# Kernel optimization log

Measured on AMD Instinct MI355X. Metric: run time of the kernel, lower is better.

## Reference

```python
import jax, jax.numpy as jnp
import numpy as np

WS = 7
HEADS = 8
DIM = 256
IN_DIM = 128
HID = 1024
EPS = 1e-5


def _rel_index(ws):
    coords = np.stack(np.meshgrid(np.arange(ws), np.arange(ws), indexing='ij'))  # (2,ws,ws)
    cf = coords.reshape(2, -1)                      # (2,N)
    rel = (cf[:, :, None] - cf[:, None, :]).transpose(1, 2, 0).copy()  # (N,N,2)
    rel[..., 0] += ws - 1
    rel[..., 1] += ws - 1
    rel[..., 0] *= 2 * ws - 1
    return rel.sum(-1)  # (N,N) int

REL_IDX = jnp.asarray(_rel_index(WS).reshape(-1))


def layernorm(x, g, b):
    mu = jnp.mean(x, axis=-1, keepdims=True)
    var = jnp.mean(jnp.square(x - mu), axis=-1, keepdims=True)
    return (x - mu) * jax.lax.rsqrt(var + EPS) * g + b


def setup_inputs() -> dict:
    key = jax.random.key(0)
    ks = jax.random.split(key, 16)
    s = 0.02
    return {
        'x': jax.random.normal(ks[0], (16, IN_DIM, 56, 56), jnp.float32),
        'conv_w': jax.random.normal(ks[1], (DIM, IN_DIM, 3, 3), jnp.float32) * s,
        'conv_b': jnp.zeros((DIM,), jnp.float32),
        'g1': jnp.ones((DIM,), jnp.float32), 'b1': jnp.zeros((DIM,), jnp.float32),
        'g2': jnp.ones((DIM,), jnp.float32), 'b2': jnp.zeros((DIM,), jnp.float32),
        'g3': jnp.ones((DIM,), jnp.float32), 'b3': jnp.zeros((DIM,), jnp.float32),
        'qkv_w': jax.random.normal(ks[2], (3 * DIM, DIM), jnp.float32) * s,
        'rel_bias_table': jax.random.normal(ks[3], ((2 * WS - 1) ** 2, HEADS), jnp.float32) * s,
        'proj_w': jax.random.normal(ks[4], (DIM, DIM), jnp.float32) * s,
        'proj_b': jnp.zeros((DIM,), jnp.float32),
        'fc1_w': jax.random.normal(ks[5], (HID, DIM), jnp.float32) * s,
        'fc1_b': jnp.zeros((HID,), jnp.float32),
        'fc2_w': jax.random.normal(ks[6], (DIM, HID), jnp.float32) * s,
        'fc2_b': jnp.zeros((DIM,), jnp.float32),
    }


def reference(x, conv_w, conv_b, g1, b1, g2, b2, g3, b3, qkv_w, rel_bias_table,
              proj_w, proj_b, fc1_w, fc1_b, fc2_w, fc2_b):
    # proj_q: 3x3 conv, stride 1, pad 1 (input_dim != embed_dim)
    x = jax.lax.conv_general_dilated(
        x, conv_w, window_strides=(1, 1), padding=((1, 1), (1, 1)),
        dimension_numbers=('NCHW', 'OIHW', 'NCHW')) + conv_b[None, :, None, None]
    b, c, h, w = x.shape
    x = x.reshape(b, c, h * w).transpose(0, 2, 1)  # (b, n, c)
    x = layernorm(x, g1, b1)
    x = x.reshape(b, h, w, c)
    pb = (WS - h % WS) % WS
    pr = (WS - w % WS) % WS
    x = jnp.pad(x, ((0, 0), (0, pb), (0, pr), (0, 0)))
    hp, wp = h + pb, w + pr
    # window partition -> (nW, N, c)
    xw = x.reshape(b, hp // WS, WS, wp // WS, WS, c)
    xw = xw.transpose(0, 1, 3, 2, 4, 5).reshape(-1, WS * WS, c)
    nW, N, _ = xw.shape
    d = c // HEADS
    qkv = (xw @ qkv_w.T).reshape(nW, N, 3, HEADS, d).transpose(2, 0, 3, 1, 4)  # (3,nW,h,N,d)
    q, k, v = qkv[0] * (d ** -0.5), qkv[1], qkv[2]
    attn = jnp.einsum('whnd,whmd->whnm', q, k)
    bias = rel_bias_table[REL_IDX].reshape(N, N, HEADS).transpose(2, 0, 1)  # (h,N,N)
    attn = jax.nn.softmax(attn + bias[None], axis=-1)
    out = jnp.einsum('whnm,whmd->whnd', attn, v).transpose(0, 2, 1, 3).reshape(nW, N, c)
    out = out @ proj_w.T + proj_b
    # window reverse
    x = out.reshape(b, hp // WS, wp // WS, WS, WS, c)
    x = x.transpose(0, 1, 3, 2, 4, 5).reshape(b, hp, wp, c)
    x = x[:, :h, :w, :].reshape(b, h * w, c)
    # NOTE: faithful to source — NO residual from pre-attention stream
    x = layernorm(x, g2, b2)
    x = jax.nn.gelu(x @ fc1_w.T + fc1_b, approximate=False) @ fc2_w.T + fc2_b
    x = x + x  # source: x = x + drop_path(x) with identity drop_path
    x = layernorm(x, g3, b3)
    return x.reshape(b, h, w, c).transpose(0, 3, 1, 2)
```

## Files before the change

### kernel.cpp

```cpp
#include <hip/hip_runtime.h>
#include <hip/hip_bf16.h>

typedef unsigned short u16;
typedef unsigned int   u32;

#define TTOK  50176
#define CDIM  256

using short8 = __attribute__((ext_vector_type(8))) short;
using f32x4  = __attribute__((ext_vector_type(4))) float;

__device__ __forceinline__ float b2f(u16 u) { return __uint_as_float(((u32)u) << 16); }
__device__ __forceinline__ u16 f2b(float f) {
    u32 x = __float_as_uint(f);
    return (u16)((x + 0x7fffu + ((x >> 16) & 1u)) >> 16);
}

#define GLD16(src, dst) __builtin_amdgcn_global_load_lds( \
    (const __attribute__((address_space(1))) void*)(src),  \
    (__attribute__((address_space(3))) void*)(dst), 16, 0, 0)

__global__ __launch_bounds__(256) void cvt4_k(const float* __restrict__ a, const float* __restrict__ b,
                                              const float* __restrict__ c, const float* __restrict__ d,
                                              u16* __restrict__ dst) {
    int i = blockIdx.x * 256 + threadIdx.x;
    const float* src; int off;
    if (i < 49152)       { src = a; off = i; }
    else if (i < 65536)  { src = b; off = i - 49152; }
    else if (i < 131072) { src = c; off = i - 65536; }
    else                 { src = d; off = i - 131072; }
    float4 v = *(const float4*)&src[off * 4];
    ushort4 o;
    o.x = f2b(v.x); o.y = f2b(v.y); o.z = f2b(v.z); o.w = f2b(v.w);
    *(ushort4*)&dst[i * 4] = o;
}

__global__ __launch_bounds__(256) void pad_k(const float* __restrict__ x, u16* __restrict__ xp) {
    __shared__ float tile[128][58];
    int bid = blockIdx.x;
    int b = bid / 58, hp = bid - b * 58;
    int tid = threadIdx.x;
    bool zrow = (hp == 0 || hp == 57);
    if (!zrow) {
        int h = hp - 1;
        for (int e = tid; e < 128 * 14; e += 256) {
            int ic = e / 14, j = e - ic * 14;
            float4 v = *(const float4*)&x[(((size_t)b * 128 + ic) * 56 + h) * 56 + j * 4];
            tile[ic][j * 4 + 0] = v.x; tile[ic][j * 4 + 1] = v.y;
            tile[ic][j * 4 + 2] = v.z; tile[ic][j * 4 + 3] = v.w;
        }
        __syncthreads();
    }
    size_t rb = ((size_t)b * 58 + hp) * 58 * 128;
    for (int u = tid; u < 58 * 16; u += 256) {
        int wp = u / 16, icg = u - wp * 16;
        uint4 o = make_uint4(0u, 0u, 0u, 0u);
        if (!zrow && wp != 0 && wp != 57) {
            int w = wp - 1, ic0 = icg * 8;
            u16 v0 = f2b(tile[ic0 + 0][w]), v1 = f2b(tile[ic0 + 1][w]);
            u16 v2 = f2b(tile[ic0 + 2][w]), v3 = f2b(tile[ic0 + 3][w]);
            u16 v4 = f2b(tile[ic0 + 4][w]), v5 = f2b(tile[ic0 + 5][w]);
            u16 v6 = f2b(tile[ic0 + 6][w]), v7 = f2b(tile[ic0 + 7][w]);
            o.x = (u32)v0 | ((u32)v1 << 16);
            o.y = (u32)v2 | ((u32)v3 << 16);
            o.z = (u32)v4 | ((u32)v5 << 16);
            o.w = (u32)v6 | ((u32)v7 << 16);
        }
        *(uint4*)&xp[rb + (size_t)wp * 128 + icg * 8] = o;
    }
}

__global__ __launch_bounds__(256) void w2_k(const float* __restrict__ w, u16* __restrict__ o2) {
    int e = blockIdx.x * 256 + threadIdx.x;
    int o = e / 1152, rem = e - o * 1152;
    int tap = rem >> 7, ic = rem & 127;
    o2[e] = f2b(w[(o * 128 + ic) * 9 + tap]);
}

__device__ __forceinline__ void xcd_remap(int& bx, int& by) {
    int nx = gridDim.x, ny = gridDim.y;
    if ((ny & 7) == 0) {
        int linear = blockIdx.y * nx + blockIdx.x;
        int xcd = linear & 7, within = linear >> 3;
        bx = within % nx;
        by = xcd * (ny >> 3) + within / nx;
    } else { bx = blockIdx.x; by = blockIdx.y; }
}

__device__ __forceinline__ int xcd_remap1d() {
    int nb = gridDim.x, lin = blockIdx.x;
    int q = nb >> 3, r = nb & 7;
    int xcd = lin & 7, idx = lin >> 3;
    return (xcd < r ? xcd * (q + 1) : r * (q + 1) + (xcd - r) * q) + idx;
}

__global__ __launch_bounds__(256) void gemm_conv_ln_k(const u16* __restrict__ xp, const u16* __restrict__ W2,
                                                      const float* __restrict__ bias,
                                                      const float* __restrict__ gam, const float* __restrict__ bet,
                                                      u16* __restrict__ C) {
    __shared__ __align__(16) u16 lsA[64 * 64];
    __shared__ __align__(16) u16 lsB[256 * 64];
    int tid = threadIdx.x;
    int wave = tid >> 6, lane = tid & 63;
    int by = xcd_remap1d();
    int mBase = by * 64;
    int wm = wave >> 1, wn = wave & 1;
    int lr = lane & 15, lq = lane >> 4;
    int r8 = lane >> 3, kg = lane & 7;
    int kgsw = ((kg ^ r8) & 7) * 8;

    size_t tb[2]; const u16* gB[8];
#pragma unroll
    for (int j = 0; j < 2; ++j) {
        int t = mBase + wave * 16 + j * 8 + r8;
        int win = t / 49, n = t - win * 49;
        int b = win >> 6, wh = (win >> 3) & 7, ww = win & 7;
        int r = n / 7, s = n - r * 7;
        tb[j] = ((size_t)(b * 58 + wh * 7 + r) * 58 + ww * 7 + s) * 128 + kgsw;
    }
#pragma unroll
    for (int j = 0; j < 8; ++j)
        gB[j] = W2 + (size_t)(wave * 64 + j * 8 + r8) * 1152 + kgsw;

    f32x4 acc[2][8];
#pragma unroll
    for (int m = 0; m < 2; ++m)
#pragma unroll
        for (int n = 0; n < 8; ++n) acc[m][n] = (f32x4){0.f, 0.f, 0.f, 0.f};

    for (int ks = 0; ks < 18; ++ks) {
        int tap = ks >> 1, half = ks & 1;
        int kh = tap / 3, kw = tap - kh * 3;
        int uoff = (kh * 58 + kw) * 128 + half * 64;
#pragma unroll
        for (int j = 0; j < 2; ++j) GLD16(xp + tb[j] + uoff, lsA + (wave * 16 + j * 8) * 64);
#pragma unroll
        for (int j = 0; j < 8; ++j) GLD16(gB[j] + ks * 64, lsB + (wave * 64 + j * 8) * 64);
        __syncthreads();
#pragma unroll
        for (int kk = 0; kk < 2; ++kk) {
            int sl = (((kk << 2) | lq) ^ (lr & 7)) * 8;
            short8 af[2], bf[8];
#pragma unroll
            for (int m = 0; m < 2; ++m)
                af[m] = *(const short8*)&lsA[(wm * 32 + m * 16 + lr) * 64 + sl];
#pragma unroll
            for (int n = 0; n < 8; ++n)
                bf[n] = *(const short8*)&lsB[(wn * 128 + n * 16 + lr) * 64 + sl];
#pragma unroll
            for (int m = 0; m < 2; ++m)
#pragma unroll
                for (int n = 0; n < 8; ++n)
                    acc[m][n] = __builtin_amdgcn_mfma_f32_16x16x32_bf16(af[m], bf[n], acc[m][n], 0, 0, 0);
        }
        __syncthreads();
    }

    float bv[8], gv[8], btv[8];
#pragma unroll
    for (int n = 0; n < 8; ++n) {
        int col = wn * 128 + n * 16 + lr;
        bv[n] = bias[col]; gv[n] = gam[col]; btv[n] = bet[col];
    }
#pragma unroll
    for (int m = 0; m < 2; ++m)
#pragma unroll
        for (int n = 0; n < 8; ++n)
#pragma unroll
            for (int r = 0; r < 4; ++r) acc[m][n][r] += bv[n];

    float* red = (float*)lsA;
#pragma unroll
    for (int m = 0; m < 2; ++m)
#pragma unroll
        for (int r = 0; r < 4; ++r) {
            float s = 0.f, qq = 0.f;
#pragma unroll
            for (int n = 0; n < 8; ++n) { float v = acc[m][n][r]; s += v; qq += v * v; }
            s += __shfl_xor(s, 1); s += __shfl_xor(s, 2); s += __shfl_xor(s, 4); s += __shfl_xor(s, 8);
            qq += __shfl_xor(qq, 1); qq += __shfl_xor(qq, 2); qq += __shfl_xor(qq, 4); qq += __shfl_xor(qq, 8);
            if (lr == 0) {
                int row = wm * 32 + m * 16 + lq * 4 + r;
                red[row * 4 + wn * 2] = s; red[row * 4 + wn * 2 + 1] = qq;
            }
        }
    __syncthreads();

#pragma unroll
    for (int m = 0; m < 2; ++m)
#pragma unroll
        for (int r = 0; r < 4; ++r) {
            int row = wm * 32 + m * 16 + lq * 4 + r;
            float S = red[row * 4] + red[row * 4 + 2];
            float Q = red[row * 4 + 1] + red[row * 4 + 3];
            float mean = S * (1.f / 256.f);
            float var = Q * (1.f / 256.f) - mean * mean;
            float inv = rsqrtf(var + 1e-5f);
            size_t grow = (size_t)(mBase + row) * 256;
#pragma unroll
            for (int n = 0; n < 8; ++n) {
                int col = wn * 128 + n * 16 + lr;
                C[grow + col] = f2b((acc[m][n][r] - mean) * inv * gv[n] + btv[n]);
            }
        }
}

__global__ __launch_bounds__(256) void gemm_ln_k(const u16* __restrict__ A, const u16* __restrict__ Bw,
                                                 const float* __restrict__ bias,
                                                 const float* __restrict__ gam, const float* __restrict__ bet,
                                                 u16* __restrict__ C, int K) {
    __shared__ __align__(16) u16 lsA[64 * 64];
    __shared__ __align__(16) u16 lsB[256 * 64];
    int tid = threadIdx.x;
    int wave = tid >> 6, lane = tid & 63;
    int by = xcd_remap1d();
    int mBase = by * 64;
    int wm = wave >> 1, wn = wave & 1;
    int lr = lane & 15, lq = lane >> 4;
    int r8 = lane >> 3, kg = lane & 7;
    int kgsw = ((kg ^ r8) & 7) * 8;

    const u16* gA[2]; const u16* gB[8];
#pragma unroll
    for (int j = 0; j < 2; ++j)
        gA[j] = A + (size_t)(mBase + wave * 16 + j * 8 + r8) * K + kgsw;
#pragma unroll
    for (int j = 0; j < 8; ++j)
        gB[j] = Bw + (size_t)(wave * 64 + j * 8 + r8) * K + kgsw;

    f32x4 acc[2][8];
#pragma unroll
    for (int m = 0; m < 2; ++m)
#pragma unroll
        for (int n = 0; n < 8; ++n) acc[m][n] = (f32x4){0.f, 0.f, 0.f, 0.f};

    for (int k0 = 0; k0 < K; k0 += 64) {
#pragma unroll
        for (int j = 0; j < 2; ++j) GLD16(gA[j] + k0, lsA + (wave * 16 + j * 8) * 64);
#pragma unroll
        for (int j = 0; j < 8; ++j) GLD16(gB[j] + k0, lsB + (wave * 64 + j * 8) * 64);
        __syncthreads();
#pragma unroll
        for (int kk = 0; kk < 2; ++kk) {
            int sl = (((kk << 2) | lq) ^ (lr & 7)) * 8;
            short8 af[2], bf[8];
#pragma unroll
            for (int m = 0; m < 2; ++m)
                af[m] = *(const short8*)&lsA[(wm * 32 + m * 16 + lr) * 64 + sl];
#pragma unroll
            for (int n = 0; n < 8; ++n)
                bf[n] = *(const short8*)&lsB[(wn * 128 + n * 16 + lr) * 64 + sl];
#pragma unroll
            for (int m = 0; m < 2; ++m)
#pragma unroll
                for (int n = 0; n < 8; ++n)
                    acc[m][n] = __builtin_amdgcn_mfma_f32_16x16x32_bf16(af[m], bf[n], acc[m][n], 0, 0, 0);
        }
        __syncthreads();
    }

    float bv[8], gv[8], btv[8];
#pragma unroll
    for (int n = 0; n < 8; ++n) {
        int col = wn * 128 + n * 16 + lr;
        bv[n] = bias[col]; gv[n] = gam[col]; btv[n] = bet[col];
    }
#pragma unroll
    for (int m = 0; m < 2; ++m)
#pragma unroll
        for (int n = 0; n < 8; ++n)
#pragma unroll
            for (int r = 0; r < 4; ++r) acc[m][n][r] += bv[n];

    float* red = (float*)lsA;
#pragma unroll
    for (int m = 0; m < 2; ++m)
#pragma unroll
        for (int r = 0; r < 4; ++r) {
            float s = 0.f, qq = 0.f;
#pragma unroll
            for (int n = 0; n < 8; ++n) { float v = acc[m][n][r]; s += v; qq += v * v; }
            s += __shfl_xor(s, 1); s += __shfl_xor(s, 2); s += __shfl_xor(s, 4); s += __shfl_xor(s, 8);
            qq += __shfl_xor(qq, 1); qq += __shfl_xor(qq, 2); qq += __shfl_xor(qq, 4); qq += __shfl_xor(qq, 8);
            if (lr == 0) {
                int row = wm * 32 + m * 16 + lq * 4 + r;
                red[row * 4 + wn * 2] = s; red[row * 4 + wn * 2 + 1] = qq;
            }
        }
    __syncthreads();

#pragma unroll
    for (int m = 0; m < 2; ++m)
#pragma unroll
        for (int r = 0; r < 4; ++r) {
            int row = wm * 32 + m * 16 + lq * 4 + r;
            float S = red[row * 4] + red[row * 4 + 2];
            float Q = red[row * 4 + 1] + red[row * 4 + 3];
            float mean = S * (1.f / 256.f);
            float var = Q * (1.f / 256.f) - mean * mean;
            float inv = rsqrtf(var + 1e-5f);
            size_t grow = (size_t)(mBase + row) * 256;
#pragma unroll
            for (int n = 0; n < 8; ++n) {
                int col = wn * 128 + n * 16 + lr;
                C[grow + col] = f2b((acc[m][n][r] - mean) * inv * gv[n] + btv[n]);
            }
        }
}

template <int EPI>
__global__ __launch_bounds__(256) void gemm_k(const u16* __restrict__ A, const u16* __restrict__ Bw,
                                              const float* __restrict__ bias, u16* __restrict__ C,
                                              int M, int N, int K) {
    __shared__ __align__(16) u16 lsA[128 * 64];
    __shared__ __align__(16) u16 lsB[128 * 64];
    int tid = threadIdx.x;
    int wave = tid >> 6, lane = tid & 63;
    int bx, by; xcd_remap(bx, by);
    int mBase = by * 128, nBase = bx * 128;
    int wm = wave >> 1, wn = wave & 1;
    int lr = lane & 15, lq = lane >> 4;
    int r8 = lane >> 3, kg = lane & 7;
    int kgsw = ((kg ^ r8) & 7) * 8;

    const u16* gA[4]; const u16* gB[4];
#pragma unroll
    for (int i = 0; i < 4; ++i) {
        int crow = wave * 4 + i;
        gA[i] = A  + (size_t)(mBase + crow * 8 + r8) * K + kgsw;
        gB[i] = Bw + (size_t)(nBase + crow * 8 + r8) * K + kgsw;
    }

    f32x4 acc[4][4];
#pragma unroll
    for (int m = 0; m < 4; ++m)
#pragma unroll
        for (int n = 0; n < 4; ++n) acc[m][n] = (f32x4){0.f, 0.f, 0.f, 0.f};

    for (int k0 = 0; k0 < K; k0 += 64) {
#pragma unroll
        for (int i = 0; i < 4; ++i) {
            int crow = wave * 4 + i;
            GLD16(gA[i] + k0, lsA + crow * 512);
            GLD16(gB[i] + k0, lsB + crow * 512);
        }
        __syncthreads();
#pragma unroll
        for (int kk = 0; kk < 2; ++kk) {
            int sl = (((kk << 2) | lq) ^ (lr & 7)) * 8;
            short8 af[4], bf[4];
#pragma unroll
            for (int m = 0; m < 4; ++m)
                af[m] = *(const short8*)&lsA[(wm * 64 + m * 16 + lr) * 64 + sl];
#pragma unroll
            for (int n = 0; n < 4; ++n)
                bf[n] = *(const short8*)&lsB[(wn * 64 + n * 16 + lr) * 64 + sl];
#pragma unroll
            for (int m = 0; m < 4; ++m)
#pragma unroll
                for (int n = 0; n < 4; ++n)
                    acc[m][n] = __builtin_amdgcn_mfma_f32_16x16x32_bf16(af[m], bf[n], acc[m][n], 0, 0, 0);
        }
        __syncthreads();
    }

#pragma unroll
    for (int m = 0; m < 4; ++m) {
        int row0 = mBase + wm * 64 + m * 16 + lq * 4;
#pragma unroll
        for (int n = 0; n < 4; ++n) {
            int col = nBase + wn * 64 + n * 16 + lr;
            float bv = (EPI >= 1) ? bias[col] : 0.f;
#pragma unroll
            for (int r = 0; r < 4; ++r) {
                float v = acc[m][n][r] + bv;
                if (EPI == 2) {
                    float u = 0.79788456f * (v + 0.044715f * v * v * v);
                    float e = __expf(-2.f * u);
                    v = v * __frcp_rn(1.f + e);
                }
                C[(size_t)(row0 + r) * N + col] = f2b(v);
            }
        }
    }
}

__global__ __launch_bounds__(256) void attn_mfma_k(const u16* __restrict__ qkv,
                                                   const float* __restrict__ tab,
                                                   u16* __restrict__ out) {
    __shared__ __align__(16) u16 sh[28488];
    int tid = threadIdx.x;
    int wave = tid >> 6, lane = tid & 63;
    int wh = blockIdx.x * 4 + wave;
    int win = wh >> 3, head = wh & 7;
    int g = lane >> 4, cc = lane & 15;

    u16* Pl = sh + wave * 4608;
    u16* Vl = sh + 18432 + wave * 2176;
    float* bs = (float*)(sh + 27136) + wave * 169;

    const size_t wbase = (size_t)win * 49 * 768;
    for (int e = lane; e < 169; e += 64) bs[e] = tab[e * 8 + head];
    for (int e = lane; e < 49 * 16; e += 64) {
        int k = e >> 4, d0 = (e & 15) * 2;
        *(u32*)&Vl[k * 34 + d0] = *(const u32*)&qkv[wbase + (size_t)k * 768 + 512 + head * 32 + d0];
    }
    for (int e = lane; e < 15 * 16; e += 64) {
        int k = 49 + (e >> 4), d0 = (e & 15) * 2;
        *(u32*)&Vl[k * 34 + d0] = 0u;
    }
    __syncthreads();

    short8 aQ[4], bK[4];
#pragma unroll
    for (int t = 0; t < 4; ++t) {
        int qr = t * 16 + cc; if (qr > 48) qr = 48;
        aQ[t] = *(const short8*)&qkv[wbase + (size_t)qr * 768 + head * 32 + g * 8];
        int kr = t * 16 + cc; if (kr > 48) kr = 48;
        bK[t] = *(const short8*)&qkv[wbase + (size_t)kr * 768 + 256 + head * 32 + g * 8];
    }
    f32x4 S[4][4];
#pragma unroll
    for (int a = 0; a < 4; ++a)
#pragma unroll
        for (int b = 0; b < 4; ++b)
            S[a][b] = __builtin_amdgcn_mfma_f32_16x16x32_bf16(aQ[a], bK[b], (f32x4){0.f,0.f,0.f,0.f}, 0, 0, 0);

    int AqA[4][4];
#pragma unroll
    for (int tr = 0; tr < 4; ++tr)
#pragma unroll
        for (int r = 0; r < 4; ++r) {
            int q = tr * 16 + g * 4 + r; if (q > 48) q = 48;
            int dq = (q * 37) >> 8;
            AqA[tr][r] = 6 * dq + q + 84;
        }
    int AcA[4];
    bool colBad[4];
#pragma unroll
    for (int tc = 0; tc < 4; ++tc) {
        int c = tc * 16 + cc;
        colBad[tc] = (c > 48);
        if (c > 48) c = 48;
        int dc = (c * 37) >> 8;
        AcA[tc] = 6 * dc + c;
    }
    const float scale = 0.17677669529663687f;
    float inv[4][4];
#pragma unroll
    for (int tr = 0; tr < 4; ++tr) {
#pragma unroll
        for (int r = 0; r < 4; ++r) {
            float z0 = colBad[0] ? -1e30f : S[tr][0][r] * scale + bs[AqA[tr][r] - AcA[0]];
            float z1 = colBad[1] ? -1e30f : S[tr][1][r] * scale + bs[AqA[tr][r] - AcA[1]];
            float z2 = colBad[2] ? -1e30f : S[tr][2][r] * scale + bs[AqA[tr][r] - AcA[2]];
            float z3 = colBad[3] ? -1e30f : S[tr][3][r] * scale + bs[AqA[tr][r] - AcA[3]];
            float mx = fmaxf(fmaxf(z0, z1), fmaxf(z2, z3));
            mx = fmaxf(mx, __shfl_xor(mx, 1));
            mx = fmaxf(mx, __shfl_xor(mx, 2));
            mx = fmaxf(mx, __shfl_xor(mx, 4));
            mx = fmaxf(mx, __shfl_xor(mx, 8));
            float p0 = __expf(z0 - mx), p1 = __expf(z1 - mx);
            float p2 = __expf(z2 - mx), p3 = __expf(z3 - mx);
            S[tr][0][r] = p0; S[tr][1][r] = p1; S[tr][2][r] = p2; S[tr][3][r] = p3;
            float sm = p0 + p1 + p2 + p3;
            sm += __shfl_xor(sm, 1); sm += __shfl_xor(sm, 2);
            sm += __shfl_xor(sm, 4); sm += __shfl_xor(sm, 8);
            inv[tr][r] = 1.0f / sm;
        }
    }

#pragma unroll
    for (int tr = 0; tr < 4; ++tr)
#pragma unroll
        for (int tc = 0; tc < 4; ++tc) {
            int k = tc * 16 + cc;
            u16* pb = &Pl[tr * 1152 + k * 18 + g * 4];
            u32 w0 = (u32)f2b(S[tr][tc][0]) | ((u32)f2b(S[tr][tc][1]) << 16);
            u32 w1 = (u32)f2b(S[tr][tc][2]) | ((u32)f2b(S[tr][tc][3]) << 16);
            *(u32*)pb = w0;
            *(u32*)(pb + 2) = w1;
        }
    __syncthreads();

    f32x4 O[4][2];
#pragma unroll
    for (int a = 0; a < 4; ++a) { O[a][0] = (f32x4){0.f,0.f,0.f,0.f}; O[a][1] = (f32x4){0.f,0.f,0.f,0.f}; }
#pragma unroll
    for (int s = 0; s < 2; ++s) {
        short8 pa[4], vb[2];
#pragma unroll
        for (int tr = 0; tr < 4; ++tr)
#pragma unroll
            for (int j = 0; j < 8; ++j)
                pa[tr][j] = (short)Pl[tr * 1152 + (s * 32 + g * 8 + j) * 18 + cc];
#pragma unroll
        for (int td = 0; td < 2; ++td)
#pragma unroll
            for (int j = 0; j < 8; ++j)
                vb[td][j] = (short)Vl[(s * 32 + g * 8 + j) * 34 + td * 16 + cc];
#pragma unroll
        for (int tr = 0; tr < 4; ++tr)
#pragma unroll
            for (int td = 0; td < 2; ++td)
                O[tr][td] = __builtin_amdgcn_mfma_f32_16x16x32_bf16(pa[tr], vb[td], O[tr][td], 0, 0, 0);
    }

#pragma unroll
    for (int tr = 0; tr < 4; ++tr)
#pragma unroll
        for (int r = 0; r < 4; ++r) {
            int q = tr * 16 + g * 4 + r;
            if (q < 49) {
                float iv = inv[tr][r];
                u16* op = out + (size_t)(win * 49 + q) * 256 + head * 32;
                op[cc]      = f2b(O[tr][0][r] * iv);
                op[16 + cc] = f2b(O[tr][1][r] * iv);
            }
        }
}

__global__ __launch_bounds__(256) void ln3_out_k(const u16* __restrict__ f, const float* __restrict__ g3,
                                                 const float* __restrict__ b3, float* __restrict__ out) {
    __shared__ float tile[256][57];
    int bh = blockIdx.x;
    int b = bh / 56, h = bh - b * 56;
    int wv = threadIdx.x >> 6, lane = threadIdx.x & 63;
    int wh = h / 7, r = h - wh * 7;
    float4 gg = *(const float4*)&g3[lane * 4];
    float4 bb = *(const float4*)&b3[lane * 4];
    for (int i = 0; i < 14; ++i) {
        int w = wv + i * 4;
        int wwn = w / 7, s2 = w - wwn * 7;
        int t = (b * 64 + wh * 8 + wwn) * 49 + r * 7 + s2;
        ushort4 u = *(const ushort4*)&f[(size_t)t * 256 + lane * 4];
        float v0 = 2.f * b2f(u.x), v1 = 2.f * b2f(u.y), v2 = 2.f * b2f(u.z), v3 = 2.f * b2f(u.w);
        float s = v0 + v1 + v2 + v3;
        float q = v0 * v0 + v1 * v1 + v2 * v2 + v3 * v3;
#pragma unroll
        for (int o = 32; o; o >>= 1) { s += __shfl_xor(s, o); q += __shfl_xor(q, o); }
        float mean = s * (1.f / 256.f);
        float var = q * (1.f / 256.f) - mean * mean;
        float inv = rsqrtf(var + 1e-5f);
        int c = lane * 4;
        tile[c + 0][w] = (v0 - mean) * inv * gg.x + bb.x;
        tile[c + 1][w] = (v1 - mean) * inv * gg.y + bb.y;
        tile[c + 2][w] = (v2 - mean) * inv * gg.z + bb.z;
        tile[c + 3][w] = (v3 - mean) * inv * gg.w + bb.w;
    }
    __syncthreads();
    size_t obase = (size_t)b * 256 * 3136 + (size_t)h * 56;
#pragma unroll
    for (int it = 0; it < 28; ++it) {
        int e = it * 256 + threadIdx.x;
        int c = e / 28, wu = e - c * 28;
        float2 pack = make_float2(tile[c][wu * 2], tile[c][wu * 2 + 1]);
        *(float2*)&out[obase + (size_t)c * 3136 + wu * 2] = pack;
    }
}

extern "C" void kernel_launch(void* const* d_in, const int* in_sizes, int n_in,
                              void* d_out, int out_size, void* d_ws, size_t ws_size,
                              hipStream_t stream) {
    (void)in_sizes; (void)n_in; (void)out_size;
    const float* x      = (const float*)d_in[0];
    const float* conv_w = (const float*)d_in[1];
    const float* conv_b = (const float*)d_in[2];
    const float* g1     = (const float*)d_in[3];
    const float* b1     = (const float*)d_in[4];
    const float* g2     = (const float*)d_in[5];
    const float* b2     = (const float*)d_in[6];
    const float* g3     = (const float*)d_in[7];
    const float* b3     = (const float*)d_in[8];
    const float* qkv_w  = (const float*)d_in[9];
    const float* tab    = (const float*)d_in[10];
    const float* proj_w = (const float*)d_in[11];
    const float* proj_b = (const float*)d_in[12];
    const float* fc1_w  = (const float*)d_in[13];
    const float* fc1_b  = (const float*)d_in[14];
    const float* fc2_w  = (const float*)d_in[15];
    const float* fc2_b  = (const float*)d_in[16];
    float* outp = (float*)d_out;

    const size_t OFF_Y  = (size_t)TTOK * 1152 * 2;
    const size_t OFF_AT = OFF_Y + (size_t)TTOK * 512;
    const size_t NEED   = OFF_AT + (size_t)TTOK * 512;
    if (ws_size < NEED) return;

    char* ws = (char*)d_ws;
    u16* xpad    = (u16*)ws;
    u16* ybuf    = (u16*)(ws + OFF_Y);
    u16* atout   = (u16*)(ws + OFF_AT);
    u16* qkvbuf  = (u16*)ws;
    u16* hidden  = (u16*)ws;
    u16* W2      = atout;
    u16* wbase   = (u16*)(ws + (size_t)TTOK * 1024 * 2);
    u16* qkvw_b  = wbase;
    u16* projw_b = wbase + 196608;
    u16* fc1w_b  = projw_b + 65536;
    u16* fc2w_b  = fc1w_b + 262144;

    pad_k<<<928, 256, 0, stream>>>(x, xpad);
    w2_k<<<1152, 256, 0, stream>>>(conv_w, W2);
    cvt4_k<<<768, 256, 0, stream>>>(qkv_w, proj_w, fc1_w, fc2_w, qkvw_b);
    gemm_conv_ln_k<<<784, 256, 0, stream>>>(xpad, W2, conv_b, g1, b1, ybuf);
    gemm_k<0><<<dim3(6, 392), 256, 0, stream>>>(ybuf, qkvw_b, nullptr, qkvbuf, TTOK, 768, 256);
    attn_mfma_k<<<2048, 256, 0, stream>>>(qkvbuf, tab, atout);
    gemm_ln_k<<<784, 256, 0, stream>>>(atout, projw_b, proj_b, g2, b2, ybuf, 256);
    gemm_k<2><<<dim3(8, 392), 256, 0, stream>>>(ybuf, fc1w_b, fc1_b, hidden, TTOK, 1024, 256);
    gemm_k<1><<<dim3(2, 392), 256, 0, stream>>>(hidden, fc2w_b, fc2_b, atout, TTOK, 256, 1024);
    ln3_out_k<<<896, 256, 0, stream>>>(atout, g3, b3, outp);
}
```

Before: 328.8 us.

## Fuse fc1+GELU+fc2 MLP into one kernel keeping hidden activations in LDS

Replaces the two MLP GEMM launches with a single kernel. Each block owns 64 rows, computes fc1 in 128-column chunks, applies bias and GELU, stores the chunk in swizzled LDS, and accumulates fc2 immediately. This removes the round trip of the 50176x1024 bf16 hidden tensor through global memory. The cost is that weight fragments are read straight from global/L2 with no LDS staging, and each block has a small 64-row tile with more accumulator registers. The GELU remains the tanh approximation, and the EPI==2 path is removed from the generic GEMM.

```diff
diff --git a/kernel.cpp b/kernel.cpp
--- a/kernel.cpp
+++ b/kernel.cpp
@@ -374,15 +374,115 @@
 #pragma unroll
             for (int r = 0; r < 4; ++r) {
                 float v = acc[m][n][r] + bv;
-                if (EPI == 2) {
+                C[(size_t)(row0 + r) * N + col] = f2b(v);
+            }
+        }
+    }
+}
+
+__global__ __launch_bounds__(256) void mlp_k(const u16* __restrict__ A, const u16* __restrict__ W1,
+                                             const float* __restrict__ b1v, const u16* __restrict__ W2,
+                                             const float* __restrict__ b2v, u16* __restrict__ C) {
+    __shared__ __align__(16) u16 lsA[4 * 64 * 64];
+    __shared__ __align__(16) u16 lsH[2 * 64 * 64];
+    int tid = threadIdx.x;
+    int wave = tid >> 6, lane = tid & 63;
+    int mBase = blockIdx.x * 64;
+    int wm = wave >> 1, wn = wave & 1;
+    int lr = lane & 15, lq = lane >> 4;
+    int r8 = lane >> 3, kg = lane & 7;
+    int kgsw = ((kg ^ r8) & 7) * 8;
+
+#pragma unroll
+    for (int s = 0; s < 4; ++s)
+#pragma unroll
+        for (int i = 0; i < 2; ++i) {
+            int row = wave * 8 + i * 32 + r8;
+            GLD16(A + (size_t)(mBase + row) * 256 + s * 64 + kgsw,
+                  lsA + (s * 64 + i * 32 + wave * 8) * 64);
+        }
+    __syncthreads();
+
+    f32x4 acc2[2][8];
+#pragma unroll
+    for (int m = 0; m < 2; ++m)
+#pragma unroll
+        for (int n = 0; n < 8; ++n) acc2[m][n] = (f32x4){0.f, 0.f, 0.f, 0.f};
+
+    for (int hc = 0; hc < 8; ++hc) {
+        f32x4 a1[2][4];
+#pragma unroll
+        for (int m = 0; m < 2; ++m)
+#pragma unroll
+            for (int n = 0; n < 4; ++n) a1[m][n] = (f32x4){0.f, 0.f, 0.f, 0.f};
+#pragma unroll
+        for (int ks = 0; ks < 8; ++ks) {
+            int s = ks >> 1, kk = ks & 1;
+            int sl = (((kk << 2) | lq) ^ (lr & 7)) * 8;
+            short8 af[2], bf[4];
+#pragma unroll
+            for (int m = 0; m < 2; ++m)
+                af[m] = *(const short8*)&lsA[(s * 64 + wm * 32 + m * 16 + lr) * 64 + sl];
+#pragma unroll
+            for (int n = 0; n < 4; ++n)
+                bf[n] = *(const short8*)&W1[(size_t)(hc * 128 + wn * 64 + n * 16 + lr) * 256 + ks * 32 + lq * 8];
+#pragma unroll
+            for (int m = 0; m < 2; ++m)
+#pragma unroll
+                for (int n = 0; n < 4; ++n)
+                    a1[m][n] = __builtin_amdgcn_mfma_f32_16x16x32_bf16(af[m], bf[n], a1[m][n], 0, 0, 0);
+        }
+        float bb[4];
+#pragma unroll
+        for (int n = 0; n < 4; ++n) bb[n] = b1v[hc * 128 + wn * 64 + n * 16 + lr];
+#pragma unroll
+        for (int m = 0; m < 2; ++m)
+#pragma unroll
+            for (int n = 0; n < 4; ++n) {
+                int kin = n * 16 + lr, g8 = kin >> 3, j = kin & 7;
+#pragma unroll
+                for (int rr = 0; rr < 4; ++rr) {
+                    int row = wm * 32 + m * 16 + lq * 4 + rr;
+                    float v = a1[m][n][rr] + bb[n];
                     float u = 0.79788456f * (v + 0.044715f * v * v * v);
                     float e = __expf(-2.f * u);
                     v = v * __frcp_rn(1.f + e);
+                    lsH[wn * 4096 + row * 64 + (((u32)g8 ^ ((u32)row & 7u)) << 3) + j] = f2b(v);
                 }
-                C[(size_t)(row0 + r) * N + col] = f2b(v);
             }
-        }
-    }
+        __syncthreads();
+#pragma unroll
+        for (int t = 0; t < 4; ++t) {
+            int sub = t >> 1, kk2 = t & 1;
+            int sl = (((kk2 << 2) | lq) ^ (lr & 7)) * 8;
+            short8 af2[2], bf2[8];
+#pragma unroll
+            for (int m = 0; m < 2; ++m)
+                af2[m] = *(const short8*)&lsH[(sub * 64 + wm * 32 + m * 16 + lr) * 64 + sl];
+#pragma unroll
+            for (int n = 0; n < 8; ++n)
+                bf2[n] = *(const short8*)&W2[(size_t)(wn * 128 + n * 16 + lr) * 1024 + hc * 128 + sub * 64 + kk2 * 32 + lq * 8];
+#pragma unroll
+            for (int m = 0; m < 2; ++m)
+#pragma unroll
+                for (int n = 0; n < 8; ++n)
+                    acc2[m][n] = __builtin_amdgcn_mfma_f32_16x16x32_bf16(af2[m], bf2[n], acc2[m][n], 0, 0, 0);
+        }
+        __syncthreads();
+    }
+
+#pragma unroll
+    for (int m = 0; m < 2; ++m)
+#pragma unroll
+        for (int n = 0; n < 8; ++n) {
+            int col = wn * 128 + n * 16 + lr;
+            float bv = b2v[col];
+#pragma unroll
+            for (int rr = 0; rr < 4; ++rr) {
+                int row = mBase + wm * 32 + m * 16 + lq * 4 + rr;
+                C[(size_t)row * 256 + col] = f2b(acc2[m][n][rr] + bv);
+            }
+        }
 }
 
 __global__ __launch_bounds__(256) void attn_mfma_k(const u16* __restrict__ qkv,
@@ -592,7 +692,6 @@
     u16* ybuf    = (u16*)(ws + OFF_Y);
     u16* atout   = (u16*)(ws + OFF_AT);
     u16* qkvbuf  = (u16*)ws;
-    u16* hidden  = (u16*)ws;
     u16* W2      = atout;
     u16* wbase   = (u16*)(ws + (size_t)TTOK * 1024 * 2);
     u16* qkvw_b  = wbase;
@@ -607,7 +706,6 @@
     gemm_k<0><<<dim3(6, 392), 256, 0, stream>>>(ybuf, qkvw_b, nullptr, qkvbuf, TTOK, 768, 256);
     attn_mfma_k<<<2048, 256, 0, stream>>>(qkvbuf, tab, atout);
     gemm_ln_k<<<784, 256, 0, stream>>>(atout, projw_b, proj_b, g2, b2, ybuf, 256);
-    gemm_k<2><<<dim3(8, 392), 256, 0, stream>>>(ybuf, fc1w_b, fc1_b, hidden, TTOK, 1024, 256);
-    gemm_k<1><<<dim3(2, 392), 256, 0, stream>>>(hidden, fc2w_b, fc2_b, atout, TTOK, 256, 1024);
+    mlp_k<<<784, 256, 0, stream>>>(ybuf, fc1w_b, fc1_b, fc2w_b, fc2_b, atout);
     ln3_out_k<<<896, 256, 0, stream>>>(atout, g3, b3, outp);
 }
```

Result: slower. 523.4 us (+59.2%).

## Double-buffer LDS tiles in generic GEMM with K-step of 32

Applied to the files above, without the earlier changes.

Restructures the generic bf16 GEMM kernel to use two LDS buffers of 128x32 per operand. The next K-slice is loaded with global_load_lds while MFMAs run on the current one, and the swizzle is reworked for the narrower tile. This aims to hide global-load latency behind compute, at the cost of twice as many K iterations and barriers per tile.

```diff
diff --git a/kernel.cpp b/kernel.cpp
--- a/kernel.cpp
+++ b/kernel.cpp
@@ -312,23 +312,23 @@
 __global__ __launch_bounds__(256) void gemm_k(const u16* __restrict__ A, const u16* __restrict__ Bw,
                                               const float* __restrict__ bias, u16* __restrict__ C,
                                               int M, int N, int K) {
-    __shared__ __align__(16) u16 lsA[128 * 64];
-    __shared__ __align__(16) u16 lsB[128 * 64];
+    __shared__ __align__(16) u16 lsA[2][128 * 32];
+    __shared__ __align__(16) u16 lsB[2][128 * 32];
     int tid = threadIdx.x;
     int wave = tid >> 6, lane = tid & 63;
     int bx, by; xcd_remap(bx, by);
     int mBase = by * 128, nBase = bx * 128;
     int wm = wave >> 1, wn = wave & 1;
     int lr = lane & 15, lq = lane >> 4;
-    int r8 = lane >> 3, kg = lane & 7;
-    int kgsw = ((kg ^ r8) & 7) * 8;
-
-    const u16* gA[4]; const u16* gB[4];
-#pragma unroll
-    for (int i = 0; i < 4; ++i) {
-        int crow = wave * 4 + i;
-        gA[i] = A  + (size_t)(mBase + crow * 8 + r8) * K + kgsw;
-        gB[i] = Bw + (size_t)(nBase + crow * 8 + r8) * K + kgsw;
+    int rr = lane >> 2, kc = lane & 3;
+    int kcs = (kc ^ ((rr >> 1) & 3)) * 8;
+
+    const u16* gA[2]; const u16* gB[2];
+#pragma unroll
+    for (int j = 0; j < 2; ++j) {
+        int row = wave * 32 + j * 16 + rr;
+        gA[j] = A  + (size_t)(mBase + row) * K + kcs;
+        gB[j] = Bw + (size_t)(nBase + row) * K + kcs;
     }
 
     f32x4 acc[4][4];
@@ -337,30 +337,38 @@
 #pragma unroll
         for (int n = 0; n < 4; ++n) acc[m][n] = (f32x4){0.f, 0.f, 0.f, 0.f};
 
-    for (int k0 = 0; k0 < K; k0 += 64) {
-#pragma unroll
-        for (int i = 0; i < 4; ++i) {
-            int crow = wave * 4 + i;
-            GLD16(gA[i] + k0, lsA + crow * 512);
-            GLD16(gB[i] + k0, lsB + crow * 512);
-        }
-        __syncthreads();
-#pragma unroll
-        for (int kk = 0; kk < 2; ++kk) {
-            int sl = (((kk << 2) | lq) ^ (lr & 7)) * 8;
-            short8 af[4], bf[4];
-#pragma unroll
-            for (int m = 0; m < 4; ++m)
-                af[m] = *(const short8*)&lsA[(wm * 64 + m * 16 + lr) * 64 + sl];
+    int nk = K >> 5;
+#pragma unroll
+    for (int j = 0; j < 2; ++j) {
+        GLD16(gA[j], &lsA[0][(wave * 32 + j * 16) * 32]);
+        GLD16(gB[j], &lsB[0][(wave * 32 + j * 16) * 32]);
+    }
+    __syncthreads();
+
+    int slq = (lq ^ ((lr >> 1) & 3)) * 8;
+    for (int ks = 0; ks < nk; ++ks) {
+        int cur = ks & 1;
+        if (ks + 1 < nk) {
+            int nxt = cur ^ 1;
+            int ko = (ks + 1) << 5;
+#pragma unroll
+            for (int j = 0; j < 2; ++j) {
+                GLD16(gA[j] + ko, &lsA[nxt][(wave * 32 + j * 16) * 32]);
+                GLD16(gB[j] + ko, &lsB[nxt][(wave * 32 + j * 16) * 32]);
+            }
+        }
+        short8 af[4], bf[4];
+#pragma unroll
+        for (int m = 0; m < 4; ++m)
+            af[m] = *(const short8*)&lsA[cur][(wm * 64 + m * 16 + lr) * 32 + slq];
+#pragma unroll
+        for (int n = 0; n < 4; ++n)
+            bf[n] = *(const short8*)&lsB[cur][(wn * 64 + n * 16 + lr) * 32 + slq];
+#pragma unroll
+        for (int m = 0; m < 4; ++m)
 #pragma unroll
             for (int n = 0; n < 4; ++n)
-                bf[n] = *(const short8*)&lsB[(wn * 64 + n * 16 + lr) * 64 + sl];
-#pragma unroll
-            for (int m = 0; m < 4; ++m)
-#pragma unroll
-                for (int n = 0; n < 4; ++n)
-                    acc[m][n] = __builtin_amdgcn_mfma_f32_16x16x32_bf16(af[m], bf[n], acc[m][n], 0, 0, 0);
-        }
+                acc[m][n] = __builtin_amdgcn_mfma_f32_16x16x32_bf16(af[m], bf[n], acc[m][n], 0, 0, 0);
         __syncthreads();
     }
 
```

New measurement: 326.1 us. Within noise of the previous version (-0.8%).
